# Optimization experiments

Measured on AMD Instinct MI355X. Metric: run time of the kernel, lower is better.

Reference implementation:

```python
import jax, jax.numpy as jnp
import numpy as np

THETA = 1.0
DILATIONS = (1, 2, 3, 4)
EPS = 1e-6


def _scale_features(x, d):
    # x: [B, C, H, W]; one pyramid scale (dilation d)
    B, C, H, W = x.shape
    k = 3 + 2 * (d - 1)          # kernel size per original formula
    pad = d * d                   # pad so effective span d*(k-1)+1 = 2d^2+1 preserves HxW
    K = k * k
    patches = jax.lax.conv_general_dilated_patches(
        x, (k, k), (1, 1), [(pad, pad), (pad, pad)], rhs_dilation=(d, d)
    )  # [B, C*K, H, W], channel-major per input channel
    p = patches.reshape(B, C, K, H, W)

    mu = p.mean(axis=2, keepdims=True)
    diff = p - mu
    var_biased = (diff * diff).mean(axis=2)                 # E[(p-mu)^2]
    std = jnp.sqrt(var_biased * (K / (K - 1))) + EPS        # torch .std is unbiased (ddof=1)

    contrast = var_biased / (std * std)                     # mean(normed^2)
    energy = (p * p).mean(axis=2)
    entropy = -(p * jnp.log(p + EPS)).mean(axis=2)
    # NB: original precedence -> 1.0 / mean(1 + |p - mu|)
    homogeneity = 1.0 / ((1.0 + jnp.abs(diff)).mean(axis=2))

    feats = jnp.stack([contrast, energy, entropy, homogeneity], axis=2)  # [B, C, 4, H, W]
    # martingale transform: exp(theta*log(f+eps) - 0.5*theta^2)
    M = jnp.exp(THETA * jnp.log(feats + EPS) - 0.5 * THETA ** 2)
    return M.reshape(B, C * 4, H, W)  # cat over channels of per-channel feature stacks


def setup_inputs() -> dict:
    key = jax.random.key(0)
    x = jax.random.uniform(key, (2, 4, 256, 256), dtype=jnp.float32)
    return {"x": x}


def reference(x):
    return tuple(_scale_features(x, d) for d in DILATIONS)
```

## Files before the change

### kernel.cpp

```cpp
#include <hip/hip_runtime.h>
#include <cstddef>

#define EPS 1e-6f
constexpr float INV_SQRT_E = 0.6065306597126334f;

template <int D>
__device__ __forceinline__ void body(const float* __restrict__ x,
                                     float* __restrict__ out,
                                     char* smem, int bc, int H, int W)
{
    constexpr int PAD = D * D;
    constexpr int KS  = 2 * D + 1;
    constexpr int K   = KS * KS;
    constexpr int TW  = 64, TH = 8;
    constexpr int LW  = TW + 2 * PAD;
    constexpr int LH  = TH + 2 * PAD;
    constexpr float INVK = 1.0f / (float)K;
    constexpr float UNB  = (float)K / (float)(K - 1);

    float2* sv  = (float2*)smem;
    float2* cs2 = (float2*)(smem + LH * LW * 8);
    float*  cs1 = (float*) (smem + LH * LW * 8 + TH * LW * 8);

    const int w0 = blockIdx.x * TW;
    const int h0 = blockIdx.y * TH;
    const float* xp = x + (size_t)bc * H * W;

    const int tid = threadIdx.y * 64 + threadIdx.x;
    for (int idx = tid; idx < LH * LW; idx += 512) {
        const int r  = idx / LW;
        const int cc = idx - r * LW;
        const int gh = h0 - PAD + r;
        const int gw = w0 - PAD + cc;
        float v = 0.0f;
        if (gh >= 0 && gh < H && gw >= 0 && gw < W) v = xp[gh * W + gw];
        sv[idx] = make_float2(v, v * __logf(v + EPS));
    }
    __syncthreads();

    const int tx = threadIdx.x;
    const int ty = threadIdx.y;

    float s = 0.0f, s2 = 0.0f, sl = 0.0f;
    float sad;

    if constexpr (K <= 9) {
        const float2* base = &sv[ty * LW + tx];
        float ta[K];
        #pragma unroll
        for (int mi = 0; mi < KS; ++mi)
            #pragma unroll
            for (int mj = 0; mj < KS; ++mj) {
                const float2 p = base[(mi * D) * LW + mj * D];
                ta[mi * KS + mj] = p.x;
                s  += p.x;
                s2  = fmaf(p.x, p.x, s2);
                sl += p.y;
            }
        const float mu = s * INVK;
        sad = 0.0f;
        #pragma unroll
        for (int i = 0; i < K; ++i) sad += fabsf(ta[i] - mu);
    } else {
        for (int e = tid; e < TH * LW; e += 512) {
            const int r = e / LW;
            const int c = e - r * LW;
            const float2* cp = &sv[r * LW + c];
            float vs = 0.0f, vs2 = 0.0f, vsl = 0.0f;
            #pragma unroll
            for (int mi = 0; mi < KS; ++mi) {
                const float2 p = cp[(mi * D) * LW];
                vs  += p.x;
                vs2  = fmaf(p.x, p.x, vs2);
                vsl += p.y;
            }
            cs2[e] = make_float2(vs, vs2);
            cs1[e] = vsl;
        }
        __syncthreads();

        const float2* q2 = &cs2[ty * LW + tx];
        const float*  q1 = &cs1[ty * LW + tx];
        #pragma unroll
        for (int mj = 0; mj < KS; ++mj) {
            const float2 q = q2[mj * D];
            s  += q.x;
            s2 += q.y;
            sl += q1[mj * D];
        }
        const float mu = s * INVK;

        const float2* base = &sv[ty * LW + tx];
        sad = 0.0f;
        #pragma unroll
        for (int mi = 0; mi < KS; ++mi)
            #pragma unroll
            for (int mj = 0; mj < KS; ++mj)
                sad += fabsf(base[(mi * D) * LW + mj * D].x - mu);
    }

    const float mu       = s * INVK;
    const float energy   = s2 * INVK;
    const float var      = fmaxf(energy - mu * mu, 0.0f);
    const float sd       = sqrtf(var * UNB) + EPS;
    const float contrast = var / (sd * sd);
    const float entropy  = -sl * INVK;
    const float homog    = 1.0f / (1.0f + sad * INVK);

    const size_t fstride = (size_t)H * W;
    const size_t rowoff  = (size_t)(h0 + ty) * W;
    float* op = out + (size_t)bc * 4 * fstride + w0 + tx;
    __builtin_nontemporal_store((contrast + EPS) * INV_SQRT_E, &op[0 * fstride + rowoff]);
    __builtin_nontemporal_store((energy   + EPS) * INV_SQRT_E, &op[1 * fstride + rowoff]);
    __builtin_nontemporal_store((entropy  + EPS) * INV_SQRT_E, &op[2 * fstride + rowoff]);
    __builtin_nontemporal_store((homog    + EPS) * INV_SQRT_E, &op[3 * fstride + rowoff]);
}

__global__ __launch_bounds__(512, 8) void tex_fused(
    const float* __restrict__ x, float* __restrict__ out, int H, int W)
{
    extern __shared__ char smem[];
    const int dz = blockIdx.z >> 3;
    const int bc = blockIdx.z & 7;
    const size_t per = (size_t)8 * 4 * H * W;
    switch (dz) {
        case 0: body<4>(x, out + 3 * per, smem, bc, H, W); break;
        case 1: body<3>(x, out + 2 * per, smem, bc, H, W); break;
        case 2: body<2>(x, out + 1 * per, smem, bc, H, W); break;
        default: body<1>(x, out + 0 * per, smem, bc, H, W); break;
    }
}

extern "C" void kernel_launch(void* const* d_in, const int* in_sizes, int n_in,
                              void* d_out, int out_size, void* d_ws, size_t ws_size,
                              hipStream_t stream) {
    const float* x = (const float*)d_in[0];
    float* out = (float*)d_out;

    const int H = 256, W = 256;
    const size_t smem_bytes = 39936;

    dim3 blk(64, 8, 1);
    dim3 grd(W / 64, H / 8, 8 * 4);
    tex_fused<<<grd, blk, smem_bytes, stream>>>(x, out, H, W);
}
```

Measured before the change: 79.67 us.

## Compute two output rows per thread and share SAD loads between row pairs

Doubles the tile height so each thread produces two output rows. The rows are paired D apart so their dilated windows overlap, letting one pass over the shared loads feed both absolute-deviation sums. It also applies the column-sum precomputation to every dilation, packed into float4, and halves the grid. This cuts per-output shared-memory reads and block count, at the cost of more shared memory (61 KB), lower occupancy bounds and a special case for D=3.

```diff
diff --git a/kernel.cpp b/kernel.cpp
--- a/kernel.cpp
+++ b/kernel.cpp
@@ -12,21 +12,20 @@
     constexpr int PAD = D * D;
     constexpr int KS  = 2 * D + 1;
     constexpr int K   = KS * KS;
-    constexpr int TW  = 64, TH = 8;
+    constexpr int TW  = 64, TH = 16;
     constexpr int LW  = TW + 2 * PAD;
     constexpr int LH  = TH + 2 * PAD;
     constexpr float INVK = 1.0f / (float)K;
     constexpr float UNB  = (float)K / (float)(K - 1);
 
-    float2* sv  = (float2*)smem;
-    float2* cs2 = (float2*)(smem + LH * LW * 8);
-    float*  cs1 = (float*) (smem + LH * LW * 8 + TH * LW * 8);
+    float2* sv = (float2*)smem;
+    float4* cs = (float4*)(smem + LH * LW * 8);
 
     const int w0 = blockIdx.x * TW;
     const int h0 = blockIdx.y * TH;
     const float* xp = x + (size_t)bc * H * W;
+    const int tid = threadIdx.y * 64 + threadIdx.x;
 
-    const int tid = threadIdx.y * 64 + threadIdx.x;
     for (int idx = tid; idx < LH * LW; idx += 512) {
         const int r  = idx / LW;
         const int cc = idx - r * LW;
@@ -38,85 +37,95 @@
     }
     __syncthreads();
 
-    const int tx = threadIdx.x;
-    const int ty = threadIdx.y;
+    for (int e = tid; e < TH * LW; e += 512) {
+        const int r = e / LW;
+        const int c = e - r * LW;
+        const float2* cp = &sv[r * LW + c];
+        float vs = 0.0f, vs2 = 0.0f, vsl = 0.0f;
+        #pragma unroll
+        for (int mi = 0; mi < KS; ++mi) {
+            const float2 p = cp[(mi * D) * LW];
+            vs  += p.x;
+            vs2  = fmaf(p.x, p.x, vs2);
+            vsl += p.y;
+        }
+        cs[e] = make_float4(vs, vs2, vsl, 0.0f);
+    }
+    __syncthreads();
 
-    float s = 0.0f, s2 = 0.0f, sl = 0.0f;
-    float sad;
+    const int tx = threadIdx.x, ty = threadIdx.y;
 
-    if constexpr (K <= 9) {
-        const float2* base = &sv[ty * LW + tx];
-        float ta[K];
+    int g = ty / D, u = ty - g * D;
+    int ra = 2 * D * g + u, rb = ra + D;
+    bool shared_pair = true;
+    if constexpr (D == 3) {
+        if (ty == 7) { ra = 13; rb = 14; shared_pair = false; }
+    }
+
+    float sa = 0, s2a = 0, sla = 0, sb = 0, s2b = 0, slb = 0;
+    {
+        const float4* qa = &cs[ra * LW + tx];
+        const float4* qb = &cs[rb * LW + tx];
+        #pragma unroll
+        for (int mj = 0; mj < KS; ++mj) {
+            const float4 A = qa[mj * D];
+            const float4 B = qb[mj * D];
+            sa += A.x; s2a += A.y; sla += A.z;
+            sb += B.x; s2b += B.y; slb += B.z;
+        }
+    }
+    const float mua = sa * INVK, mub = sb * INVK;
+
+    float sada = 0.0f, sadb = 0.0f;
+    const float2* basea = &sv[ra * LW + tx];
+    if (shared_pair) {
+        #pragma unroll
+        for (int mj = 0; mj < KS; ++mj) {
+            #pragma unroll
+            for (int t = 0; t <= KS; ++t) {
+                const float v = basea[(t * D) * LW + mj * D].x;
+                if (t < KS)  sada += fabsf(v - mua);
+                if (t >= 1)  sadb += fabsf(v - mub);
+            }
+        }
+    } else {
+        const float2* baseb = &sv[rb * LW + tx];
         #pragma unroll
         for (int mi = 0; mi < KS; ++mi)
             #pragma unroll
             for (int mj = 0; mj < KS; ++mj) {
-                const float2 p = base[(mi * D) * LW + mj * D];
-                ta[mi * KS + mj] = p.x;
-                s  += p.x;
-                s2  = fmaf(p.x, p.x, s2);
-                sl += p.y;
+                sada += fabsf(basea[(mi * D) * LW + mj * D].x - mua);
+                sadb += fabsf(baseb[(mi * D) * LW + mj * D].x - mub);
             }
-        const float mu = s * INVK;
-        sad = 0.0f;
-        #pragma unroll
-        for (int i = 0; i < K; ++i) sad += fabsf(ta[i] - mu);
-    } else {
-        for (int e = tid; e < TH * LW; e += 512) {
-            const int r = e / LW;
-            const int c = e - r * LW;
-            const float2* cp = &sv[r * LW + c];
-            float vs = 0.0f, vs2 = 0.0f, vsl = 0.0f;
-            #pragma unroll
-            for (int mi = 0; mi < KS; ++mi) {
-                const float2 p = cp[(mi * D) * LW];
-                vs  += p.x;
-                vs2  = fmaf(p.x, p.x, vs2);
-                vsl += p.y;
-            }
-            cs2[e] = make_float2(vs, vs2);
-            cs1[e] = vsl;
-        }
-        __syncthreads();
-
-        const float2* q2 = &cs2[ty * LW + tx];
-        const float*  q1 = &cs1[ty * LW + tx];
-        #pragma unroll
-        for (int mj = 0; mj < KS; ++mj) {
-            const float2 q = q2[mj * D];
-            s  += q.x;
-            s2 += q.y;
-            sl += q1[mj * D];
-        }
-        const float mu = s * INVK;
-
-        const float2* base = &sv[ty * LW + tx];
-        sad = 0.0f;
-        #pragma unroll
-        for (int mi = 0; mi < KS; ++mi)
-            #pragma unroll
-            for (int mj = 0; mj < KS; ++mj)
-                sad += fabsf(base[(mi * D) * LW + mj * D].x - mu);
     }
 
-    const float mu       = s * INVK;
-    const float energy   = s2 * INVK;
-    const float var      = fmaxf(energy - mu * mu, 0.0f);
-    const float sd       = sqrtf(var * UNB) + EPS;
-    const float contrast = var / (sd * sd);
-    const float entropy  = -sl * INVK;
-    const float homog    = 1.0f / (1.0f + sad * INVK);
+    const size_t fstride = (size_t)H * W;
+    float* op = out + (size_t)bc * 4 * fstride + w0 + tx;
+    #pragma unroll
+    for (int half = 0; half < 2; ++half) {
+        const int   r   = half ? rb : ra;
+        const float s   = half ? sb : sa;
+        const float s2  = half ? s2b : s2a;
+        const float sl  = half ? slb : sla;
+        const float sad = half ? sadb : sada;
 
-    const size_t fstride = (size_t)H * W;
-    const size_t rowoff  = (size_t)(h0 + ty) * W;
-    float* op = out + (size_t)bc * 4 * fstride + w0 + tx;
-    __builtin_nontemporal_store((contrast + EPS) * INV_SQRT_E, &op[0 * fstride + rowoff]);
-    __builtin_nontemporal_store((energy   + EPS) * INV_SQRT_E, &op[1 * fstride + rowoff]);
-    __builtin_nontemporal_store((entropy  + EPS) * INV_SQRT_E, &op[2 * fstride + rowoff]);
-    __builtin_nontemporal_store((homog    + EPS) * INV_SQRT_E, &op[3 * fstride + rowoff]);
+        const float mu       = s * INVK;
+        const float energy   = s2 * INVK;
+        const float var      = fmaxf(energy - mu * mu, 0.0f);
+        const float sd       = sqrtf(var * UNB) + EPS;
+        const float contrast = var / (sd * sd);
+        const float entropy  = -sl * INVK;
+        const float homog    = 1.0f / (1.0f + sad * INVK);
+
+        const size_t rowoff = (size_t)(h0 + r) * W;
+        __builtin_nontemporal_store((contrast + EPS) * INV_SQRT_E, &op[0 * fstride + rowoff]);
+        __builtin_nontemporal_store((energy   + EPS) * INV_SQRT_E, &op[1 * fstride + rowoff]);
+        __builtin_nontemporal_store((entropy  + EPS) * INV_SQRT_E, &op[2 * fstride + rowoff]);
+        __builtin_nontemporal_store((homog    + EPS) * INV_SQRT_E, &op[3 * fstride + rowoff]);
+    }
 }
 
-__global__ __launch_bounds__(512, 8) void tex_fused(
+__global__ __launch_bounds__(512, 4) void tex_fused(
     const float* __restrict__ x, float* __restrict__ out, int H, int W)
 {
     extern __shared__ char smem[];
@@ -138,9 +147,9 @@
     float* out = (float*)d_out;
 
     const int H = 256, W = 256;
-    const size_t smem_bytes = 39936;
+    const size_t smem_bytes = 61440;
 
     dim3 blk(64, 8, 1);
-    dim3 grd(W / 64, H / 8, 8 * 4);
+    dim3 grd(W / 64, H / 16, 8 * 4);
     tex_fused<<<grd, blk, smem_bytes, stream>>>(x, out, H, W);
 }
```

After: 81.56 us. 2.4% more time.

## Compute two output pixels per thread with split x/log planes and vector stores

Applied to the files above, without the earlier changes.

Each thread now produces two adjacent output columns, with the block shrunk to 256 threads. Shared memory is split into separate value and x*log(x) planes so loads can be float2/float4 vectorised, and the D=1 path reuses overlapping window values between the two pixels. Outputs are written as 2-wide nontemporal stores, and the blockIdx.z mapping is interleaved so different dilations mix across the grid. Per-thread register pressure and ILP increase, and unaligned odd-offset reads fall back to scalar loads.

```diff
diff --git a/kernel.cpp b/kernel.cpp
--- a/kernel.cpp
+++ b/kernel.cpp
@@ -3,6 +3,7 @@
 
 #define EPS 1e-6f
 constexpr float INV_SQRT_E = 0.6065306597126334f;
+typedef float v2f __attribute__((ext_vector_type(2)));
 
 template <int D>
 __device__ __forceinline__ void body(const float* __restrict__ x,
@@ -15,113 +16,155 @@
     constexpr int TW  = 64, TH = 8;
     constexpr int LW  = TW + 2 * PAD;
     constexpr int LH  = TH + 2 * PAD;
+    constexpr int NE  = LH * LW;
+    constexpr int NP  = NE / 2;
     constexpr float INVK = 1.0f / (float)K;
     constexpr float UNB  = (float)K / (float)(K - 1);
 
-    float2* sv  = (float2*)smem;
-    float2* cs2 = (float2*)(smem + LH * LW * 8);
-    float*  cs1 = (float*) (smem + LH * LW * 8 + TH * LW * 8);
+    float*  sx  = (float*)smem;
+    float*  slg = sx + NE;
+    float2* cs2 = (float2*)(slg + NE);
+    float*  cs1 = (float*)(cs2 + TH * LW);
 
     const int w0 = blockIdx.x * TW;
     const int h0 = blockIdx.y * TH;
     const float* xp = x + (size_t)bc * H * W;
+    const int tid = threadIdx.y * 32 + threadIdx.x;
 
-    const int tid = threadIdx.y * 64 + threadIdx.x;
-    for (int idx = tid; idx < LH * LW; idx += 512) {
-        const int r  = idx / LW;
-        const int cc = idx - r * LW;
+    for (int e = tid; e < NP; e += 256) {
+        const int i0 = 2 * e;
+        const int r  = i0 / LW;
+        const int c  = i0 - r * LW;
         const int gh = h0 - PAD + r;
-        const int gw = w0 - PAD + cc;
-        float v = 0.0f;
-        if (gh >= 0 && gh < H && gw >= 0 && gw < W) v = xp[gh * W + gw];
-        sv[idx] = make_float2(v, v * __logf(v + EPS));
+        const int gw = w0 - PAD + c;
+        float v0 = 0.f, v1 = 0.f;
+        if (gh >= 0 && gh < H) {
+            if (gw >= 0 && gw < W)     v0 = xp[gh * W + gw];
+            if (gw + 1 >= 0 && gw + 1 < W) v1 = xp[gh * W + gw + 1];
+        }
+        *(float2*)(sx + i0)  = make_float2(v0, v1);
+        *(float2*)(slg + i0) = make_float2(v0 * __logf(v0 + EPS),
+                                           v1 * __logf(v1 + EPS));
     }
     __syncthreads();
 
-    const int tx = threadIdx.x;
-    const int ty = threadIdx.y;
+    const int tx = threadIdx.x, ty = threadIdx.y;
+    const int c0 = 2 * tx;
 
-    float s = 0.0f, s2 = 0.0f, sl = 0.0f;
-    float sad;
+    float sA, sB, s2A, s2B, slA, slB, sadA, sadB;
 
-    if constexpr (K <= 9) {
-        const float2* base = &sv[ty * LW + tx];
-        float ta[K];
+    if constexpr (D == 1) {
+        float ta[3][4];
+        sA = sB = s2A = s2B = slA = slB = 0.f;
         #pragma unroll
-        for (int mi = 0; mi < KS; ++mi)
+        for (int mi = 0; mi < 3; ++mi) {
+            const float* rp = sx  + (ty + mi) * LW + c0;
+            const float* lp = slg + (ty + mi) * LW + c0;
+            const float2 a  = *(const float2*)rp;
+            const float2 b  = *(const float2*)(rp + 2);
+            const float2 la = *(const float2*)lp;
+            const float2 lb = *(const float2*)(lp + 2);
+            ta[mi][0] = a.x; ta[mi][1] = a.y; ta[mi][2] = b.x; ta[mi][3] = b.y;
+            sA += a.x + a.y + b.x;      sB += a.y + b.x + b.y;
+            s2A = fmaf(a.x, a.x, s2A); s2A = fmaf(a.y, a.y, s2A); s2A = fmaf(b.x, b.x, s2A);
+            s2B = fmaf(a.y, a.y, s2B); s2B = fmaf(b.x, b.x, s2B); s2B = fmaf(b.y, b.y, s2B);
+            slA += la.x + la.y + lb.x;  slB += la.y + lb.x + lb.y;
+        }
+        const float muA = sA * INVK, muB = sB * INVK;
+        sadA = sadB = 0.f;
+        #pragma unroll
+        for (int mi = 0; mi < 3; ++mi)
             #pragma unroll
-            for (int mj = 0; mj < KS; ++mj) {
-                const float2 p = base[(mi * D) * LW + mj * D];
-                ta[mi * KS + mj] = p.x;
-                s  += p.x;
-                s2  = fmaf(p.x, p.x, s2);
-                sl += p.y;
+            for (int mj = 0; mj < 3; ++mj) {
+                sadA += fabsf(ta[mi][mj]     - muA);
+                sadB += fabsf(ta[mi][mj + 1] - muB);
             }
-        const float mu = s * INVK;
-        sad = 0.0f;
-        #pragma unroll
-        for (int i = 0; i < K; ++i) sad += fabsf(ta[i] - mu);
     } else {
-        for (int e = tid; e < TH * LW; e += 512) {
-            const int r = e / LW;
-            const int c = e - r * LW;
-            const float2* cp = &sv[r * LW + c];
-            float vs = 0.0f, vs2 = 0.0f, vsl = 0.0f;
+        constexpr int NCP = TH * LW / 2;
+        for (int e = tid; e < NCP; e += 256) {
+            const int i0 = 2 * e;
+            const int r  = i0 / LW;
+            const int c  = i0 - r * LW;
+            const float* cx = sx  + r * LW + c;
+            const float* cl = slg + r * LW + c;
+            float vs0 = 0, vs1 = 0, vq0 = 0, vq1 = 0, vl0 = 0, vl1 = 0;
             #pragma unroll
             for (int mi = 0; mi < KS; ++mi) {
-                const float2 p = cp[(mi * D) * LW];
-                vs  += p.x;
-                vs2  = fmaf(p.x, p.x, vs2);
-                vsl += p.y;
+                const float2 p = *(const float2*)(cx + mi * D * LW);
+                const float2 q = *(const float2*)(cl + mi * D * LW);
+                vs0 += p.x; vs1 += p.y;
+                vq0 = fmaf(p.x, p.x, vq0); vq1 = fmaf(p.y, p.y, vq1);
+                vl0 += q.x; vl1 += q.y;
             }
-            cs2[e] = make_float2(vs, vs2);
-            cs1[e] = vsl;
+            *(float4*)(cs2 + i0) = make_float4(vs0, vq0, vs1, vq1);
+            *(float2*)(cs1 + i0) = make_float2(vl0, vl1);
         }
         __syncthreads();
 
-        const float2* q2 = &cs2[ty * LW + tx];
-        const float*  q1 = &cs1[ty * LW + tx];
+        sA = sB = s2A = s2B = slA = slB = 0.f;
+        const float2* h2 = cs2 + ty * LW + c0;
+        const float*  h1 = cs1 + ty * LW + c0;
         #pragma unroll
         for (int mj = 0; mj < KS; ++mj) {
-            const float2 q = q2[mj * D];
-            s  += q.x;
-            s2 += q.y;
-            sl += q1[mj * D];
+            const int o = mj * D;
+            float2 e0, e1, l;
+            if ((o & 1) == 0) {
+                const float4 A = *(const float4*)(h2 + o);
+                e0 = make_float2(A.x, A.y); e1 = make_float2(A.z, A.w);
+                l  = *(const float2*)(h1 + o);
+            } else {
+                e0 = h2[o]; e1 = h2[o + 1];
+                l  = make_float2(h1[o], h1[o + 1]);
+            }
+            sA += e0.x; s2A += e0.y; sB += e1.x; s2B += e1.y;
+            slA += l.x; slB += l.y;
         }
-        const float mu = s * INVK;
+        const float muA = sA * INVK, muB = sB * INVK;
 
-        const float2* base = &sv[ty * LW + tx];
-        sad = 0.0f;
+        sadA = sadB = 0.f;
+        const float* bp = sx + ty * LW + c0;
         #pragma unroll
-        for (int mi = 0; mi < KS; ++mi)
+        for (int mi = 0; mi < KS; ++mi) {
+            const float* rp = bp + mi * D * LW;
             #pragma unroll
-            for (int mj = 0; mj < KS; ++mj)
-                sad += fabsf(base[(mi * D) * LW + mj * D].x - mu);
+            for (int mj = 0; mj < KS; ++mj) {
+                const int o = mj * D;
+                float2 t;
+                if ((o & 1) == 0) t = *(const float2*)(rp + o);
+                else              t = make_float2(rp[o], rp[o + 1]);
+                sadA += fabsf(t.x - muA);
+                sadB += fabsf(t.y - muB);
+            }
+        }
     }
 
-    const float mu       = s * INVK;
-    const float energy   = s2 * INVK;
-    const float var      = fmaxf(energy - mu * mu, 0.0f);
-    const float sd       = sqrtf(var * UNB) + EPS;
-    const float contrast = var / (sd * sd);
-    const float entropy  = -sl * INVK;
-    const float homog    = 1.0f / (1.0f + sad * INVK);
-
-    const size_t fstride = (size_t)H * W;
-    const size_t rowoff  = (size_t)(h0 + ty) * W;
-    float* op = out + (size_t)bc * 4 * fstride + w0 + tx;
-    __builtin_nontemporal_store((contrast + EPS) * INV_SQRT_E, &op[0 * fstride + rowoff]);
-    __builtin_nontemporal_store((energy   + EPS) * INV_SQRT_E, &op[1 * fstride + rowoff]);
-    __builtin_nontemporal_store((entropy  + EPS) * INV_SQRT_E, &op[2 * fstride + rowoff]);
-    __builtin_nontemporal_store((homog    + EPS) * INV_SQRT_E, &op[3 * fstride + rowoff]);
+    const size_t fs = (size_t)H * W;
+    const size_t ro = (size_t)(h0 + ty) * W + c0;
+    float* op = out + (size_t)bc * 4 * fs + w0;
+    const float muA = sA * INVK,  muB = sB * INVK;
+    const float enA = s2A * INVK, enB = s2B * INVK;
+    const float vaA = fmaxf(enA - muA * muA, 0.f), vaB = fmaxf(enB - muB * muB, 0.f);
+    const float sdA = sqrtf(vaA * UNB) + EPS,      sdB = sqrtf(vaB * UNB) + EPS;
+    const float coA = vaA / (sdA * sdA),           coB = vaB / (sdB * sdB);
+    const float etA = -slA * INVK,                 etB = -slB * INVK;
+    const float hoA = 1.f / (1.f + sadA * INVK),   hoB = 1.f / (1.f + sadB * INVK);
+    v2f t;
+    t = (v2f){(coA + EPS) * INV_SQRT_E, (coB + EPS) * INV_SQRT_E};
+    __builtin_nontemporal_store(t, (v2f*)(op + 0 * fs + ro));
+    t = (v2f){(enA + EPS) * INV_SQRT_E, (enB + EPS) * INV_SQRT_E};
+    __builtin_nontemporal_store(t, (v2f*)(op + 1 * fs + ro));
+    t = (v2f){(etA + EPS) * INV_SQRT_E, (etB + EPS) * INV_SQRT_E};
+    __builtin_nontemporal_store(t, (v2f*)(op + 2 * fs + ro));
+    t = (v2f){(hoA + EPS) * INV_SQRT_E, (hoB + EPS) * INV_SQRT_E};
+    __builtin_nontemporal_store(t, (v2f*)(op + 3 * fs + ro));
 }
 
-__global__ __launch_bounds__(512, 8) void tex_fused(
+__global__ __launch_bounds__(256, 4) void tex_fused(
     const float* __restrict__ x, float* __restrict__ out, int H, int W)
 {
-    extern __shared__ char smem[];
-    const int dz = blockIdx.z >> 3;
-    const int bc = blockIdx.z & 7;
+    extern __shared__ __align__(16) char smem[];
+    const int dz = blockIdx.z & 3;
+    const int bc = blockIdx.z >> 2;
     const size_t per = (size_t)8 * 4 * H * W;
     switch (dz) {
         case 0: body<4>(x, out + 3 * per, smem, bc, H, W); break;
@@ -140,7 +183,7 @@
     const int H = 256, W = 256;
     const size_t smem_bytes = 39936;
 
-    dim3 blk(64, 8, 1);
+    dim3 blk(32, 8, 1);
     dim3 grd(W / 64, H / 8, 8 * 4);
     tex_fused<<<grd, blk, smem_bytes, stream>>>(x, out, H, W);
 }
```

New measurement: 81.22 us. Within noise of the previous version (+2.0%).
